# Performance work log

Hardware: AMD Instinct MI355X
Metric: run time of the kernel (lower is better)

## Reference

```python
import jax, jax.numpy as jnp
import numpy as np

N_NODES = 50000
N_EDGES = 800000
D_IN = 256
D_HID = 256
D_OUT = 256
BN_EPS = 1e-5
NORM_EPS = 1e-12


def _glorot(key, out_dim, in_dim):
    a = np.sqrt(6.0 / (in_dim + out_dim)).astype(np.float32)
    return jax.random.uniform(key, (out_dim, in_dim), jnp.float32, -a, a)


def setup_inputs() -> dict:
    key = jax.random.key(0)
    ks = jax.random.split(key, 8)
    x = jax.random.normal(ks[0], (N_NODES, D_IN), jnp.float32)
    edge_index = jax.random.randint(ks[1], (2, N_EDGES), 0, N_NODES, dtype=jnp.int32)
    batch = jnp.zeros((N_NODES,), jnp.int32)
    return {
        "x": x,
        "W1_l": _glorot(ks[2], D_HID, D_IN),
        "b1_l": jnp.zeros((D_HID,), jnp.float32),
        "W1_r": _glorot(ks[3], D_HID, D_IN),
        "W2_l": _glorot(ks[4], D_OUT, D_HID),
        "b2_l": jnp.zeros((D_OUT,), jnp.float32),
        "W2_r": _glorot(ks[5], D_OUT, D_HID),
        "gamma1": jnp.ones((D_HID,), jnp.float32),
        "beta1": jnp.zeros((D_HID,), jnp.float32),
        "edge_index": edge_index,
        "batch": batch,
    }


def _sage_conv(x, W_l, b_l, W_r, src, dst, n_nodes):
    # PyG SAGEConv (aggr='mean'): out = lin_l(mean_j x_j) + lin_r(x)
    msgs = x[src]                                            # [E, d] gather
    s = jax.ops.segment_sum(msgs, dst, num_segments=n_nodes)  # [N, d] scatter-add
    cnt = jax.ops.segment_sum(jnp.ones((src.shape[0], 1), x.dtype), dst,
                              num_segments=n_nodes)
    agg = jnp.where(cnt > 0, s / jnp.maximum(cnt, 1.0), 0.0)
    return agg @ W_l.T + b_l + x @ W_r.T


def _batch_norm(h, gamma, beta):
    mu = jnp.mean(h, axis=0)
    var = jnp.mean((h - mu) ** 2, axis=0)  # biased, as torch train-mode BN
    return (h - mu) * jax.lax.rsqrt(var + BN_EPS) * gamma + beta


def _l2_normalize(h):
    n = jnp.linalg.norm(h, axis=-1, keepdims=True)
    return h / jnp.maximum(n, NORM_EPS)


def reference(x, W1_l, b1_l, W1_r, W2_l, b2_l, W2_r, gamma1, beta1,
              edge_index, batch):
    n = x.shape[0]
    src, dst = edge_index[0], edge_index[1]
    # layer 1: SAGEConv -> BN (train stats) -> ReLU (dropout = identity in eval)
    h = _sage_conv(x, W1_l, b1_l, W1_r, src, dst, n)
    h = jax.nn.relu(_batch_norm(h, gamma1, beta1))
    # layer 2: SAGEConv -> L2 normalize
    h = _sage_conv(h, W2_l, b2_l, W2_r, src, dst, n)
    node_emb = _l2_normalize(h)
    # global mean pool over batch ids (single graph here), then normalize
    gsum = jax.ops.segment_sum(node_emb, batch, num_segments=1)
    gcnt = jax.ops.segment_sum(jnp.ones((n, 1), node_emb.dtype), batch,
                               num_segments=1)
    graph_emb = _l2_normalize(gsum / jnp.maximum(gcnt, 1.0))
    return node_emb, graph_emb
```

## Files before the change

### kernel.cpp

```cpp
#include <hip/hip_runtime.h>
#include <math.h>

#define NN 50000
#define NE 800000
#define D  256
#define SCB 196
#define NB2 391

typedef unsigned short u16;
typedef __attribute__((ext_vector_type(8))) short short8;
typedef __attribute__((ext_vector_type(8))) unsigned short u16x8;
typedef __attribute__((ext_vector_type(4))) float f32x4;

__device__ __forceinline__ u16 f2b(float f) {
    unsigned u = __float_as_uint(f);
    return (u16)((u + 0x7FFFu + ((u >> 16) & 1u)) >> 16);
}
__device__ __forceinline__ float b2f(u16 b) {
    return __uint_as_float(((unsigned)b) << 16);
}

__device__ __forceinline__ void gl16(const u16* g, u16* l) {
    __builtin_amdgcn_global_load_lds(
        (const __attribute__((address_space(1))) void*)g,
        (__attribute__((address_space(3))) void*)l, 16, 0, 0);
}

__global__ void wxconv_kernel(const float* __restrict__ x,
                              const float* __restrict__ W1l, const float* __restrict__ W1r,
                              const float* __restrict__ W2l, const float* __restrict__ W2r,
                              const int* __restrict__ dst,
                              u16* __restrict__ Acat,
                              u16* __restrict__ Wcat1, u16* __restrict__ Wcat2,
                              int* __restrict__ deg) {
    int b = blockIdx.x;
    if (b < 12500) {
        int idx = b * 256 + threadIdx.x;
        int r = idx >> 6;
        int c4 = (idx & 63) * 4;
        float4 v = *(const float4*)&x[(size_t)r * 256 + c4];
        ushort4 o;
        o.x = f2b(v.x); o.y = f2b(v.y); o.z = f2b(v.z); o.w = f2b(v.w);
        *(ushort4*)&Acat[(size_t)r * 512 + 256 + c4] = o;
    } else if (b < 12756) {
        int r = b - 12500;
        int j = threadIdx.x;
        Wcat1[r * 512 + j]       = f2b(W1l[r * 256 + j]);
        Wcat1[r * 512 + 256 + j] = f2b(W1r[r * 256 + j]);
        Wcat2[r * 512 + j]       = f2b(W2l[r * 256 + j]);
        Wcat2[r * 512 + 256 + j] = f2b(W2r[r * 256 + j]);
    } else {
        int e0 = ((b - 12756) * 256 + threadIdx.x) * 4;
        if (e0 + 3 < NE) {
            int4 d = *(const int4*)&dst[e0];
            atomicAdd(&deg[d.x], 1);
            atomicAdd(&deg[d.y], 1);
            atomicAdd(&deg[d.z], 1);
            atomicAdd(&deg[d.w], 1);
        } else {
            for (int e = e0; e < NE; e++) atomicAdd(&deg[dst[e]], 1);
        }
    }
}

__global__ void scanA_kernel(const int* __restrict__ deg, int* __restrict__ partial) {
    int t = threadIdx.x;
    int i = blockIdx.x * 256 + t;
    int v = (i < NN) ? deg[i] : 0;
#pragma unroll
    for (int o = 32; o; o >>= 1) v += __shfl_xor(v, o);
    __shared__ int sm[4];
    if ((t & 63) == 0) sm[t >> 6] = v;
    __syncthreads();
    if (t == 0) partial[blockIdx.x] = sm[0] + sm[1] + sm[2] + sm[3];
}

__global__ void scanC_kernel(const int* __restrict__ deg, const int* __restrict__ partial,
                             int* __restrict__ offs, int* __restrict__ cur) {
    __shared__ int smp[256];
    __shared__ int sm[256];
    int t = threadIdx.x;
    int pv = (t < SCB) ? partial[t] : 0;
    smp[t] = pv;
    __syncthreads();
    for (int off = 1; off < 256; off <<= 1) {
        int u = 0;
        if (t >= off) u = smp[t - off];
        __syncthreads();
        smp[t] += u;
        __syncthreads();
    }
    int bid = blockIdx.x;
    int blockbase = (bid > 0) ? smp[bid - 1] : 0;
    if (bid == SCB - 1 && t == 255) offs[NN] = smp[255];

    int i = bid * 256 + t;
    int v = (i < NN) ? deg[i] : 0;
    sm[t] = v;
    __syncthreads();
    for (int off = 1; off < 256; off <<= 1) {
        int u = 0;
        if (t >= off) u = sm[t - off];
        __syncthreads();
        sm[t] += u;
        __syncthreads();
    }
    int o = blockbase + sm[t] - v;
    if (i < NN) {
        offs[i] = o;
        cur[i] = o;
    }
}

__global__ void fill_kernel(const int* __restrict__ src, const int* __restrict__ dst,
                            int* __restrict__ cur, int* __restrict__ csr) {
    int e0 = (blockIdx.x * blockDim.x + threadIdx.x) * 8;
    if (e0 + 7 < NE) {
        int4 d0 = *(const int4*)&dst[e0];
        int4 d1 = *(const int4*)&dst[e0 + 4];
        int4 s0 = *(const int4*)&src[e0];
        int4 s1 = *(const int4*)&src[e0 + 4];
        int p0 = atomicAdd(&cur[d0.x], 1);
        int p1 = atomicAdd(&cur[d0.y], 1);
        int p2 = atomicAdd(&cur[d0.z], 1);
        int p3 = atomicAdd(&cur[d0.w], 1);
        int p4 = atomicAdd(&cur[d1.x], 1);
        int p5 = atomicAdd(&cur[d1.y], 1);
        int p6 = atomicAdd(&cur[d1.z], 1);
        int p7 = atomicAdd(&cur[d1.w], 1);
        csr[p0] = s0.x; csr[p1] = s0.y; csr[p2] = s0.z; csr[p3] = s0.w;
        csr[p4] = s1.x; csr[p5] = s1.y; csr[p6] = s1.z; csr[p7] = s1.w;
    } else {
        for (int e = e0; e < NE; e++) {
            int pos = atomicAdd(&cur[dst[e]], 1);
            csr[pos] = src[e];
        }
    }
}

__global__ __launch_bounds__(256)
void agg_kernel(const u16* __restrict__ Acat, const int* __restrict__ csr,
                const int* __restrict__ offs, u16* __restrict__ AcatW) {
    int wid = (blockIdx.x * blockDim.x + threadIdx.x) >> 6;
    int lane = threadIdx.x & 63;
    if (wid >= NN) return;
    int beg = offs[wid];
    int end = offs[wid + 1];
    int deg = end - beg;
    int half = lane >> 5;
    int lc = (lane & 31) * 8;
    int mid = beg + ((deg + 1) >> 1);
    int e  = half ? mid : beg;
    int hi = half ? end : mid;
    float a[8] = {0.f, 0.f, 0.f, 0.f, 0.f, 0.f, 0.f, 0.f};
    for (; e + 7 < hi; e += 8) {
        int s0 = csr[e + 0], s1 = csr[e + 1], s2 = csr[e + 2], s3 = csr[e + 3];
        int s4 = csr[e + 4], s5 = csr[e + 5], s6 = csr[e + 6], s7 = csr[e + 7];
        u16x8 v0 = *(const u16x8*)&Acat[(size_t)s0 * 512 + 256 + lc];
        u16x8 v1 = *(const u16x8*)&Acat[(size_t)s1 * 512 + 256 + lc];
        u16x8 v2 = *(const u16x8*)&Acat[(size_t)s2 * 512 + 256 + lc];
        u16x8 v3 = *(const u16x8*)&Acat[(size_t)s3 * 512 + 256 + lc];
        u16x8 v4 = *(const u16x8*)&Acat[(size_t)s4 * 512 + 256 + lc];
        u16x8 v5 = *(const u16x8*)&Acat[(size_t)s5 * 512 + 256 + lc];
        u16x8 v6 = *(const u16x8*)&Acat[(size_t)s6 * 512 + 256 + lc];
        u16x8 v7 = *(const u16x8*)&Acat[(size_t)s7 * 512 + 256 + lc];
#pragma unroll
        for (int i = 0; i < 8; i++)
            a[i] += ((b2f(v0[i]) + b2f(v1[i])) + (b2f(v2[i]) + b2f(v3[i]))) +
                    ((b2f(v4[i]) + b2f(v5[i])) + (b2f(v6[i]) + b2f(v7[i])));
    }
    for (; e + 3 < hi; e += 4) {
        int s0 = csr[e + 0], s1 = csr[e + 1], s2 = csr[e + 2], s3 = csr[e + 3];
        u16x8 v0 = *(const u16x8*)&Acat[(size_t)s0 * 512 + 256 + lc];
        u16x8 v1 = *(const u16x8*)&Acat[(size_t)s1 * 512 + 256 + lc];
        u16x8 v2 = *(const u16x8*)&Acat[(size_t)s2 * 512 + 256 + lc];
        u16x8 v3 = *(const u16x8*)&Acat[(size_t)s3 * 512 + 256 + lc];
#pragma unroll
        for (int i = 0; i < 8; i++)
            a[i] += (b2f(v0[i]) + b2f(v1[i])) + (b2f(v2[i]) + b2f(v3[i]));
    }
    for (; e < hi; e++) {
        int s0 = csr[e];
        u16x8 v0 = *(const u16x8*)&Acat[(size_t)s0 * 512 + 256 + lc];
#pragma unroll
        for (int i = 0; i < 8; i++) a[i] += b2f(v0[i]);
    }
#pragma unroll
    for (int i = 0; i < 8; i++) a[i] += __shfl_xor(a[i], 32);
    float sc = (deg > 0) ? 1.0f / (float)deg : 0.0f;
    if (half == 0) {
        u16x8 o;
#pragma unroll
        for (int i = 0; i < 8; i++) o[i] = f2b(a[i] * sc);
        *(u16x8*)&AcatW[(size_t)wid * 512 + lc] = o;
    }
}

__global__ __launch_bounds__(512)
void mfma_gemm_kernel(const u16* __restrict__ A, const u16* __restrict__ W,
                      const float* __restrict__ bias, u16* __restrict__ Cout) {
    __shared__ u16 As[3][128 * 32];
    __shared__ u16 Bs[3][256 * 32];
    const int tid = threadIdx.x;
    const int l = tid & 63;
    const int wid = tid >> 6;
    const int wr = wid >> 2;
    const int wc = wid & 3;
    const int row0 = blockIdx.x * 128;

    const u16* aptr;
    const u16* bptr[2];
    {
        int row = wid * 16 + (l >> 2);
        int kg = (l & 3) ^ ((row >> 1) & 3);
        int ra = row0 + row;
        if (ra > NN - 1) ra = NN - 1;
        aptr = A + (size_t)ra * 512 + kg * 8;
    }
#pragma unroll
    for (int i = 0; i < 2; i++) {
        int row = wid * 32 + i * 16 + (l >> 2);
        int kg = (l & 3) ^ ((row >> 1) & 3);
        bptr[i] = W + (size_t)row * 512 + kg * 8;
    }

    f32x4 acc[4][4] = {};

#define STAGE1(b, t)                                                         \
    do {                                                                     \
        gl16(aptr + (t) * 32, &As[b][(wid * 16) * 32]);                      \
        _Pragma("unroll") for (int i_ = 0; i_ < 2; i_++)                     \
            gl16(bptr[i_] + (t) * 32, &Bs[b][(wid * 32 + i_ * 16) * 32]);    \
    } while (0)

    STAGE1(0, 0);
    STAGE1(1, 1);

    const int kq = l >> 4;
    const int sw = ((l & 15) >> 1) & 3;
#pragma unroll
    for (int t = 0; t < 16; t++) {
        if (t < 15) asm volatile("s_waitcnt vmcnt(3)" ::: "memory");
        else        asm volatile("s_waitcnt vmcnt(0)" ::: "memory");
        __builtin_amdgcn_s_barrier();
        __builtin_amdgcn_sched_barrier(0);

        if (t + 2 < 16) STAGE1((t + 2) % 3, t + 2);

        short8 af[4], bf[4];
#pragma unroll
        for (int m = 0; m < 4; m++) {
            int row = wr * 64 + m * 16 + (l & 15);
            af[m] = *(const short8*)&As[t % 3][row * 32 + (kq ^ sw) * 8];
        }
#pragma unroll
        for (int n = 0; n < 4; n++) {
            int row = wc * 64 + n * 16 + (l & 15);
            bf[n] = *(const short8*)&Bs[t % 3][row * 32 + (kq ^ sw) * 8];
        }
#pragma unroll
        for (int m = 0; m < 4; m++)
#pragma unroll
            for (int n = 0; n < 4; n++)
                acc[m][n] = __builtin_amdgcn_mfma_f32_16x16x32_bf16(
                    af[m], bf[n], acc[m][n], 0, 0, 0);
    }
#undef STAGE1

    const int cq = l >> 4;
    const int cc = l & 15;
#pragma unroll
    for (int m = 0; m < 4; m++) {
#pragma unroll
        for (int n = 0; n < 4; n++) {
            int c = wc * 64 + n * 16 + cc;
#pragma unroll
            for (int j = 0; j < 4; j++) {
                int r = row0 + wr * 64 + m * 16 + cq * 4 + j;
                if (r < NN)
                    Cout[(size_t)r * 256 + c] = f2b(acc[m][n][j] + bias[c]);
            }
        }
    }
}

__global__ __launch_bounds__(512)
void gemm2_l2_kernel(const u16* __restrict__ A, const u16* __restrict__ W,
                     const float* __restrict__ bias, float* __restrict__ out,
                     float* __restrict__ colsum_part) {
    __shared__ u16 As[3][128 * 32];
    __shared__ u16 Bs[3][256 * 32];
    const int tid = threadIdx.x;
    const int l = tid & 63;
    const int wid = tid >> 6;
    const int wr = wid >> 2;
    const int wc = wid & 3;
    const int row0 = blockIdx.x * 128;

    const u16* aptr;
    const u16* bptr[2];
    {
        int row = wid * 16 + (l >> 2);
        int kg = (l & 3) ^ ((row >> 1) & 3);
        int ra = row0 + row;
        if (ra > NN - 1) ra = NN - 1;
        aptr = A + (size_t)ra * 512 + kg * 8;
    }
#pragma unroll
    for (int i = 0; i < 2; i++) {
        int row = wid * 32 + i * 16 + (l >> 2);
        int kg = (l & 3) ^ ((row >> 1) & 3);
        bptr[i] = W + (size_t)row * 512 + kg * 8;
    }

    f32x4 acc[4][4] = {};

#define STAGE2(b, t)                                                         \
    do {                                                                     \
        gl16(aptr + (t) * 32, &As[b][(wid * 16) * 32]);                      \
        _Pragma("unroll") for (int i_ = 0; i_ < 2; i_++)                     \
            gl16(bptr[i_] + (t) * 32, &Bs[b][(wid * 32 + i_ * 16) * 32]);    \
    } while (0)

    STAGE2(0, 0);
    STAGE2(1, 1);

    const int kq = l >> 4;
    const int sw = ((l & 15) >> 1) & 3;
#pragma unroll
    for (int t = 0; t < 16; t++) {
        if (t < 15) asm volatile("s_waitcnt vmcnt(3)" ::: "memory");
        else        asm volatile("s_waitcnt vmcnt(0)" ::: "memory");
        __builtin_amdgcn_s_barrier();
        __builtin_amdgcn_sched_barrier(0);

        if (t + 2 < 16) STAGE2((t + 2) % 3, t + 2);

        short8 af[4], bf[4];
#pragma unroll
        for (int m = 0; m < 4; m++) {
            int row = wr * 64 + m * 16 + (l & 15);
            af[m] = *(const short8*)&As[t % 3][row * 32 + (kq ^ sw) * 8];
        }
#pragma unroll
        for (int n = 0; n < 4; n++) {
            int row = wc * 64 + n * 16 + (l & 15);
            bf[n] = *(const short8*)&Bs[t % 3][row * 32 + (kq ^ sw) * 8];
        }
#pragma unroll
        for (int m = 0; m < 4; m++)
#pragma unroll
            for (int n = 0; n < 4; n++)
                acc[m][n] = __builtin_amdgcn_mfma_f32_16x16x32_bf16(
                    af[m], bf[n], acc[m][n], 0, 0, 0);
    }
#undef STAGE2

    float* rowsq = (float*)&As[1][0];
    float* colp  = rowsq + 512;
    const int cq = l >> 4;
    const int cc = l & 15;

    float sq[4][4];
#pragma unroll
    for (int m = 0; m < 4; m++)
#pragma unroll
        for (int j = 0; j < 4; j++) {
            float s = 0.f;
#pragma unroll
            for (int n = 0; n < 4; n++) {
                float v = acc[m][n][j] + bias[wc * 64 + n * 16 + cc];
                acc[m][n][j] = v;
                s += v * v;
            }
            sq[m][j] = s;
        }
#pragma unroll
    for (int o = 1; o < 16; o <<= 1)
#pragma unroll
        for (int m = 0; m < 4; m++)
#pragma unroll
            for (int j = 0; j < 4; j++) sq[m][j] += __shfl_xor(sq[m][j], o);

    __syncthreads();
#pragma unroll
    for (int m = 0; m < 4; m++)
#pragma unroll
        for (int j = 0; j < 4; j++)
            if (cc == j) rowsq[wc * 128 + wr * 64 + m * 16 + cq * 4 + j] = sq[m][j];
    __syncthreads();

    float colpart[4] = {0.f, 0.f, 0.f, 0.f};
#pragma unroll
    for (int m = 0; m < 4; m++)
#pragma unroll
        for (int j = 0; j < 4; j++) {
            int rl = wr * 64 + m * 16 + cq * 4 + j;
            float s = rowsq[rl] + rowsq[128 + rl] + rowsq[256 + rl] + rowsq[384 + rl];
            float invn = 1.0f / fmaxf(sqrtf(s), 1e-12f);
            int r = row0 + rl;
            bool ok = (r < NN);
#pragma unroll
            for (int n = 0; n < 4; n++) {
                float vn = acc[m][n][j] * invn;
                if (ok) {
                    out[(size_t)r * 256 + wc * 64 + n * 16 + cc] = vn;
                    colpart[n] += vn;
                }
            }
        }
#pragma unroll
    for (int n = 0; n < 4; n++) {
        colpart[n] += __shfl_xor(colpart[n], 16);
        colpart[n] += __shfl_xor(colpart[n], 32);
    }
    if (l < 16) {
#pragma unroll
        for (int n = 0; n < 4; n++)
            colp[wr * 256 + wc * 64 + n * 16 + l] = colpart[n];
    }
    __syncthreads();
    if (tid < 256)
        colsum_part[(size_t)blockIdx.x * 256 + tid] = colp[tid] + colp[256 + tid];
}

__global__ __launch_bounds__(256)
void colstats_kernel(const u16* __restrict__ h, float* __restrict__ stats8) {
    __shared__ float red[8][512];
    int t = threadIdx.x;
    int cg = (t & 31) * 8;
    int rofs = t >> 5;
    float s0[8] = {}, s1[8] = {};
    for (int r = blockIdx.x * 8 + rofs; r < NN; r += gridDim.x * 8) {
        u16x8 v = *(const u16x8*)&h[(size_t)r * 256 + cg];
#pragma unroll
        for (int i = 0; i < 8; i++) {
            float f = b2f(v[i]);
            s0[i] += f;
            s1[i] += f * f;
        }
    }
#pragma unroll
    for (int i = 0; i < 8; i++) {
        red[rofs][cg + i] = s0[i];
        red[rofs][256 + cg + i] = s1[i];
    }
    __syncthreads();
    float* slot = stats8 + (blockIdx.x & 7) * 512;
    for (int k = t; k < 512; k += 256) {
        float s = red[0][k] + red[1][k] + red[2][k] + red[3][k] +
                  red[4][k] + red[5][k] + red[6][k] + red[7][k];
        atomicAdd(&slot[k], s);
    }
}

__global__ void bnrelu_kernel(const u16* __restrict__ hb,
                              const float* __restrict__ stats8,
                              const float* __restrict__ gamma,
                              const float* __restrict__ beta,
                              u16* __restrict__ Acat) {
    __shared__ float s_scale[256], s_shift[256];
    int t = threadIdx.x;
    {
        float su = 0.f, sq = 0.f;
#pragma unroll
        for (int k = 0; k < 8; k++) {
            su += stats8[k * 512 + t];
            sq += stats8[k * 512 + 256 + t];
        }
        const float invN = 1.0f / (float)NN;
        float mu = su * invN;
        float var = sq * invN - mu * mu;
        float sc = gamma[t] * rsqrtf(var + 1e-5f);
        s_scale[t] = sc;
        s_shift[t] = beta[t] - mu * sc;
    }
    __syncthreads();
    int idx = blockIdx.x * 256 + t;
    int r = idx >> 5;
    int c8 = (idx & 31) * 8;
    u16x8 v = *(const u16x8*)&hb[(size_t)r * 256 + c8];
    u16x8 o;
#pragma unroll
    for (int i = 0; i < 8; i++) {
        float f = b2f(v[i]) * s_scale[c8 + i] + s_shift[c8 + i];
        o[i] = f2b(fmaxf(f, 0.f));
    }
    *(u16x8*)&Acat[(size_t)r * 512 + 256 + c8] = o;
}

__global__ void graph_kernel(const float* __restrict__ colsum_part,
                             float* __restrict__ gout) {
    __shared__ float wsum[4];
    int j = threadIdx.x;
    float s = 0.f;
#pragma unroll 8
    for (int b = 0; b < NB2; b++) s += colsum_part[(size_t)b * 256 + j];
    float v = s * (1.0f / (float)NN);
    float sq = v * v;
#pragma unroll
    for (int o = 32; o; o >>= 1) sq += __shfl_xor(sq, o);
    if ((j & 63) == 0) wsum[j >> 6] = sq;
    __syncthreads();
    float tot = wsum[0] + wsum[1] + wsum[2] + wsum[3];
    gout[j] = v / fmaxf(sqrtf(tot), 1e-12f);
}

extern "C" void kernel_launch(void* const* d_in, const int* in_sizes, int n_in,
                              void* d_out, int out_size, void* d_ws, size_t ws_size,
                              hipStream_t stream) {
    const float* x      = (const float*)d_in[0];
    const float* W1_l   = (const float*)d_in[1];
    const float* b1_l   = (const float*)d_in[2];
    const float* W1_r   = (const float*)d_in[3];
    const float* W2_l   = (const float*)d_in[4];
    const float* b2_l   = (const float*)d_in[5];
    const float* W2_r   = (const float*)d_in[6];
    const float* gamma1 = (const float*)d_in[7];
    const float* beta1  = (const float*)d_in[8];
    const int*   eidx   = (const int*)d_in[9];
    const int* src = eidx;
    const int* dst = eidx + NE;

    char* wsb = (char*)d_ws;
    int*   deg    = (int*)(wsb + 0);
    int*   offs   = (int*)(wsb + 200000);
    int*   cur    = (int*)(wsb + 400004);
    float* stats8 = (float*)(wsb + 400004);
    int*   csr    = (int*)(wsb + 600004);
    float* cspart = (float*)(wsb + 600004);
    int*   part   = (int*)(wsb + 3800064);
    u16*   Wcat1  = (u16*)(wsb + 3807232);
    u16*   Wcat2  = (u16*)(wsb + 4069376);
    u16*   hb     = (u16*)(wsb + 4331520);
    u16*   Acat   = (u16*)(wsb + 29931520);
    float* out    = (float*)d_out;
    float* gout   = out + (size_t)NN * 256;

    hipMemsetAsync(deg, 0, NN * sizeof(int), stream);

    const int DEGB = (NE / 4 + 255) / 256;
    wxconv_kernel<<<12756 + DEGB, 256, 0, stream>>>(x, W1_l, W1_r, W2_l, W2_r,
                                                    dst, Acat, Wcat1, Wcat2, deg);

    scanA_kernel<<<SCB, 256, 0, stream>>>(deg, part);
    scanC_kernel<<<SCB, 256, 0, stream>>>(deg, part, offs, cur);
    fill_kernel<<<(NE / 8 + 255) / 256, 256, 0, stream>>>(src, dst, cur, csr);
    hipMemsetAsync(stats8, 0, 16384, stream);

    agg_kernel<<<12500, 256, 0, stream>>>(Acat, csr, offs, Acat);
    mfma_gemm_kernel<<<NB2, 512, 0, stream>>>(Acat, Wcat1, b1_l, hb);
    colstats_kernel<<<256, 256, 0, stream>>>(hb, stats8);
    bnrelu_kernel<<<6250, 256, 0, stream>>>(hb, stats8, gamma1, beta1, Acat);

    agg_kernel<<<12500, 256, 0, stream>>>(Acat, csr, offs, Acat);
    gemm2_l2_kernel<<<NB2, 512, 0, stream>>>(Acat, Wcat2, b2_l, out, cspart);

    graph_kernel<<<1, 256, 0, stream>>>(cspart, gout);
}
```

Before: 327.7 us.

## Fuse BN column statistics into GEMM1 epilogue and split GEMM1 over columns

The layer-1 GEMM now computes per-column sum and sum-of-squares from its fp32 outputs in the epilogue and writes per-block partials. A single-block kernel then reduces those partials into BN scale and shift. This removes the separate colstats pass over the bf16 hidden matrix, the stats memset and the atomics. GEMM1 also uses a 2D grid of 128x128 tiles instead of 128x256, doubling the block count to improve CU load balance, at the cost of loading the A tiles twice. The stats are now taken from the pre-rounding fp32 values, and the finalization runs on a single serial block.

```diff
diff --git a/kernel.cpp b/kernel.cpp
--- a/kernel.cpp
+++ b/kernel.cpp
@@ -197,60 +197,56 @@
 }
 
 __global__ __launch_bounds__(512)
-void mfma_gemm_kernel(const u16* __restrict__ A, const u16* __restrict__ W,
-                      const float* __restrict__ bias, u16* __restrict__ Cout) {
+void gemm1_kernel(const u16* __restrict__ A, const u16* __restrict__ W,
+                  const float* __restrict__ bias, u16* __restrict__ Cout,
+                  float* __restrict__ spart) {
     __shared__ u16 As[3][128 * 32];
-    __shared__ u16 Bs[3][256 * 32];
+    __shared__ u16 Bs[3][128 * 32];
     const int tid = threadIdx.x;
     const int l = tid & 63;
     const int wid = tid >> 6;
-    const int wr = wid >> 2;
-    const int wc = wid & 3;
+    const int wr = wid >> 1;
+    const int wc = wid & 1;
     const int row0 = blockIdx.x * 128;
+    const int col0 = blockIdx.y * 128;
 
     const u16* aptr;
-    const u16* bptr[2];
+    const u16* bptr;
     {
         int row = wid * 16 + (l >> 2);
         int kg = (l & 3) ^ ((row >> 1) & 3);
         int ra = row0 + row;
         if (ra > NN - 1) ra = NN - 1;
         aptr = A + (size_t)ra * 512 + kg * 8;
-    }
-#pragma unroll
-    for (int i = 0; i < 2; i++) {
-        int row = wid * 32 + i * 16 + (l >> 2);
-        int kg = (l & 3) ^ ((row >> 1) & 3);
-        bptr[i] = W + (size_t)row * 512 + kg * 8;
-    }
-
-    f32x4 acc[4][4] = {};
-
-#define STAGE1(b, t)                                                         \
-    do {                                                                     \
-        gl16(aptr + (t) * 32, &As[b][(wid * 16) * 32]);                      \
-        _Pragma("unroll") for (int i_ = 0; i_ < 2; i_++)                     \
-            gl16(bptr[i_] + (t) * 32, &Bs[b][(wid * 32 + i_ * 16) * 32]);    \
+        bptr = W + (size_t)(col0 + row) * 512 + kg * 8;
+    }
+
+    f32x4 acc[2][4] = {};
+
+#define STG1(b, t)                                              \
+    do {                                                        \
+        gl16(aptr + (t) * 32, &As[b][(wid * 16) * 32]);         \
+        gl16(bptr + (t) * 32, &Bs[b][(wid * 16) * 32]);         \
     } while (0)
 
-    STAGE1(0, 0);
-    STAGE1(1, 1);
+    STG1(0, 0);
+    STG1(1, 1);
 
     const int kq = l >> 4;
     const int sw = ((l & 15) >> 1) & 3;
 #pragma unroll
     for (int t = 0; t < 16; t++) {
-        if (t < 15) asm volatile("s_waitcnt vmcnt(3)" ::: "memory");
+        if (t < 15) asm volatile("s_waitcnt vmcnt(2)" ::: "memory");
         else        asm volatile("s_waitcnt vmcnt(0)" ::: "memory");
         __builtin_amdgcn_s_barrier();
         __builtin_amdgcn_sched_barrier(0);
 
-        if (t + 2 < 16) STAGE1((t + 2) % 3, t + 2);
-
-        short8 af[4], bf[4];
-#pragma unroll
-        for (int m = 0; m < 4; m++) {
-            int row = wr * 64 + m * 16 + (l & 15);
+        if (t + 2 < 16) STG1((t + 2) % 3, t + 2);
+
+        short8 af[2], bf[4];
+#pragma unroll
+        for (int m = 0; m < 2; m++) {
+            int row = wr * 32 + m * 16 + (l & 15);
             af[m] = *(const short8*)&As[t % 3][row * 32 + (kq ^ sw) * 8];
         }
 #pragma unroll
@@ -259,29 +255,77 @@
             bf[n] = *(const short8*)&Bs[t % 3][row * 32 + (kq ^ sw) * 8];
         }
 #pragma unroll
-        for (int m = 0; m < 4; m++)
+        for (int m = 0; m < 2; m++)
 #pragma unroll
             for (int n = 0; n < 4; n++)
                 acc[m][n] = __builtin_amdgcn_mfma_f32_16x16x32_bf16(
                     af[m], bf[n], acc[m][n], 0, 0, 0);
     }
-#undef STAGE1
+#undef STG1
 
     const int cq = l >> 4;
     const int cc = l & 15;
-#pragma unroll
-    for (int m = 0; m < 4; m++) {
+    float t0[4] = {0.f, 0.f, 0.f, 0.f};
+    float t1[4] = {0.f, 0.f, 0.f, 0.f};
+#pragma unroll
+    for (int m = 0; m < 2; m++) {
 #pragma unroll
         for (int n = 0; n < 4; n++) {
-            int c = wc * 64 + n * 16 + cc;
+            int c = col0 + wc * 64 + n * 16 + cc;
 #pragma unroll
             for (int j = 0; j < 4; j++) {
-                int r = row0 + wr * 64 + m * 16 + cq * 4 + j;
-                if (r < NN)
-                    Cout[(size_t)r * 256 + c] = f2b(acc[m][n][j] + bias[c]);
+                int r = row0 + wr * 32 + m * 16 + cq * 4 + j;
+                if (r < NN) {
+                    float v = acc[m][n][j] + bias[c];
+                    Cout[(size_t)r * 256 + c] = f2b(v);
+                    t0[n] += v;
+                    t1[n] += v * v;
+                }
             }
         }
     }
+#pragma unroll
+    for (int n = 0; n < 4; n++) {
+        t0[n] += __shfl_xor(t0[n], 16); t1[n] += __shfl_xor(t1[n], 16);
+        t0[n] += __shfl_xor(t0[n], 32); t1[n] += __shfl_xor(t1[n], 32);
+    }
+    __syncthreads();
+    float* sred = (float*)&As[0][0];
+    if (cq == 0) {
+#pragma unroll
+        for (int n = 0; n < 4; n++) {
+            int cl = wc * 64 + n * 16 + cc;
+            sred[wr * 256 + cl] = t0[n];
+            sred[wr * 256 + 128 + cl] = t1[n];
+        }
+    }
+    __syncthreads();
+    if (tid < 256) {
+        float s = sred[tid] + sred[256 + tid] + sred[512 + tid] + sred[768 + tid];
+        spart[(size_t)(blockIdx.x * 2 + blockIdx.y) * 256 + tid] = s;
+    }
+}
+
+__global__ void statsfin_kernel(const float* __restrict__ spart,
+                                const float* __restrict__ gamma,
+                                const float* __restrict__ beta,
+                                float* __restrict__ scale,
+                                float* __restrict__ shift) {
+    int c = threadIdx.x;
+    int by = c >> 7, cl = c & 127;
+    float su = 0.f, sq = 0.f;
+#pragma unroll 4
+    for (int bx = 0; bx < NB2; bx++) {
+        const float* p = spart + (size_t)(bx * 2 + by) * 256 + cl;
+        su += p[0];
+        sq += p[128];
+    }
+    const float invN = 1.0f / (float)NN;
+    float mu = su * invN;
+    float var = sq * invN - mu * mu;
+    float sc = gamma[c] * rsqrtf(var + 1e-5f);
+    scale[c] = sc;
+    shift[c] = beta[c] - mu * sc;
 }
 
 __global__ __launch_bounds__(512)
@@ -424,57 +468,14 @@
         colsum_part[(size_t)blockIdx.x * 256 + tid] = colp[tid] + colp[256 + tid];
 }
 
-__global__ __launch_bounds__(256)
-void colstats_kernel(const u16* __restrict__ h, float* __restrict__ stats8) {
-    __shared__ float red[8][512];
-    int t = threadIdx.x;
-    int cg = (t & 31) * 8;
-    int rofs = t >> 5;
-    float s0[8] = {}, s1[8] = {};
-    for (int r = blockIdx.x * 8 + rofs; r < NN; r += gridDim.x * 8) {
-        u16x8 v = *(const u16x8*)&h[(size_t)r * 256 + cg];
-#pragma unroll
-        for (int i = 0; i < 8; i++) {
-            float f = b2f(v[i]);
-            s0[i] += f;
-            s1[i] += f * f;
-        }
-    }
-#pragma unroll
-    for (int i = 0; i < 8; i++) {
-        red[rofs][cg + i] = s0[i];
-        red[rofs][256 + cg + i] = s1[i];
-    }
-    __syncthreads();
-    float* slot = stats8 + (blockIdx.x & 7) * 512;
-    for (int k = t; k < 512; k += 256) {
-        float s = red[0][k] + red[1][k] + red[2][k] + red[3][k] +
-                  red[4][k] + red[5][k] + red[6][k] + red[7][k];
-        atomicAdd(&slot[k], s);
-    }
-}
-
 __global__ void bnrelu_kernel(const u16* __restrict__ hb,
-                              const float* __restrict__ stats8,
-                              const float* __restrict__ gamma,
-                              const float* __restrict__ beta,
+                              const float* __restrict__ scale,
+                              const float* __restrict__ shift,
                               u16* __restrict__ Acat) {
     __shared__ float s_scale[256], s_shift[256];
     int t = threadIdx.x;
-    {
-        float su = 0.f, sq = 0.f;
-#pragma unroll
-        for (int k = 0; k < 8; k++) {
-            su += stats8[k * 512 + t];
-            sq += stats8[k * 512 + 256 + t];
-        }
-        const float invN = 1.0f / (float)NN;
-        float mu = su * invN;
-        float var = sq * invN - mu * mu;
-        float sc = gamma[t] * rsqrtf(var + 1e-5f);
-        s_scale[t] = sc;
-        s_shift[t] = beta[t] - mu * sc;
-    }
+    s_scale[t] = scale[t];
+    s_shift[t] = shift[t];
     __syncthreads();
     int idx = blockIdx.x * 256 + t;
     int r = idx >> 5;
@@ -526,14 +527,16 @@
     int*   deg    = (int*)(wsb + 0);
     int*   offs   = (int*)(wsb + 200000);
     int*   cur    = (int*)(wsb + 400004);
-    float* stats8 = (float*)(wsb + 400004);
     int*   csr    = (int*)(wsb + 600004);
     float* cspart = (float*)(wsb + 600004);
     int*   part   = (int*)(wsb + 3800064);
+    float* scale  = (float*)(wsb + 3801088);
+    float* shift  = (float*)(wsb + 3802112);
     u16*   Wcat1  = (u16*)(wsb + 3807232);
     u16*   Wcat2  = (u16*)(wsb + 4069376);
     u16*   hb     = (u16*)(wsb + 4331520);
     u16*   Acat   = (u16*)(wsb + 29931520);
+    float* spart  = (float*)(wsb + 81131520);
     float* out    = (float*)d_out;
     float* gout   = out + (size_t)NN * 256;
 
@@ -546,12 +549,12 @@
     scanA_kernel<<<SCB, 256, 0, stream>>>(deg, part);
     scanC_kernel<<<SCB, 256, 0, stream>>>(deg, part, offs, cur);
     fill_kernel<<<(NE / 8 + 255) / 256, 256, 0, stream>>>(src, dst, cur, csr);
-    hipMemsetAsync(stats8, 0, 16384, stream);
 
     agg_kernel<<<12500, 256, 0, stream>>>(Acat, csr, offs, Acat);
-    mfma_gemm_kernel<<<NB2, 512, 0, stream>>>(Acat, Wcat1, b1_l, hb);
-    colstats_kernel<<<256, 256, 0, stream>>>(hb, stats8);
-    bnrelu_kernel<<<6250, 256, 0, stream>>>(hb, stats8, gamma1, beta1, Acat);
+    dim3 g1grid(NB2, 2);
+    gemm1_kernel<<<g1grid, 512, 0, stream>>>(Acat, Wcat1, b1_l, hb, spart);
+    statsfin_kernel<<<1, 256, 0, stream>>>(spart, gamma1, beta1, scale, shift);
+    bnrelu_kernel<<<6250, 256, 0, stream>>>(hb, scale, shift, Acat);
 
     agg_kernel<<<12500, 256, 0, stream>>>(Acat, csr, offs, Acat);
     gemm2_l2_kernel<<<NB2, 512, 0, stream>>>(Acat, Wcat2, b2_l, out, cspart);
```

Result: slower. 375.1 us (+14.4%).
